# Kernel optimization log

Measured on AMD Instinct MI355X. Metric: run time of the kernel, lower is better.

## Reference

```python
import jax, jax.numpy as jnp
import numpy as np

B, S, IN, E, L = 8, 1024, 768, 256, 12

def setup_inputs() -> dict:
    key = jax.random.key(0)
    k1, k2, k3, k4 = jax.random.split(key, 4)
    input_tensor = jax.random.normal(k1, (B, S, IN), dtype=jnp.float32)
    fc_w = jax.random.normal(k2, (E, IN), dtype=jnp.float32) * (1.0 / np.sqrt(IN))
    fc_b = jax.random.normal(k3, (E,), dtype=jnp.float32) * 0.02
    bi_w = jax.random.normal(k4, (E * L, E), dtype=jnp.float32) * (1.0 / np.sqrt(E))
    bias = jnp.zeros((E,), dtype=jnp.float32)
    return {"input_tensor": input_tensor, "fc_w": fc_w, "fc_b": fc_b, "bi_w": bi_w, "bias": bias}

def reference(input_tensor, fc_w, fc_b, bi_w, bias):
    # fc: [B,S,IN] -> [B,S,E]
    t = jnp.einsum('bsi,ei->bse', input_tensor, fc_w) + fc_b
    # bi_linear: [B,S,E] -> [B,S,L,E], plus bias over E
    bl = jnp.einsum('bse,fe->bsf', t, bi_w).reshape(B, S, L, E) + bias
    # bilinear score: out[b,i,l,j] = sum_e bl[b,i,l,e] * t[b,j,e]
    # (avoids materializing the O(B*S*S*E) expanded value tensor)
    return jnp.einsum('bile,bje->bilj', bl, t)
```

## Files before the change

kernel.cpp:

```cpp
#include <hip/hip_runtime.h>
#include <hip/hip_bf16.h>

typedef __bf16 bf16_t;
typedef __bf16 bf16x8 __attribute__((ext_vector_type(8)));
typedef __bf16 bf16x4 __attribute__((ext_vector_type(4)));
typedef float f32x4 __attribute__((ext_vector_type(4)));

__global__ __launch_bounds__(256)
void cvt_all(const float* __restrict__ in, bf16_t* __restrict__ o_in,
             const float* __restrict__ fw, bf16_t* __restrict__ o_fw,
             const float* __restrict__ bw, bf16_t* __restrict__ o_bw) {
    int i = blockIdx.x * 256 + threadIdx.x;
    const float* s;
    bf16_t* d;
    int k;
    if (i < 786432)      { s = in; d = o_in; k = i; }
    else if (i < 811008) { s = fw; d = o_fw; k = i - 786432; }
    else if (i < 909312) { s = bw; d = o_bw; k = i - 811008; }
    else return;
    float4 a = ((const float4*)s)[k * 2];
    float4 b = ((const float4*)s)[k * 2 + 1];
    bf16x8 v;
    v[0] = (bf16_t)a.x; v[1] = (bf16_t)a.y; v[2] = (bf16_t)a.z; v[3] = (bf16_t)a.w;
    v[4] = (bf16_t)b.x; v[5] = (bf16_t)b.y; v[6] = (bf16_t)b.z; v[7] = (bf16_t)b.w;
    ((bf16x8*)d)[k] = v;
}

template <int BM, int BN, int EPI>
__global__ __launch_bounds__(256)
void gemm_bt(const bf16_t* __restrict__ A, const bf16_t* __restrict__ Bm,
             void* __restrict__ Cv, const float* __restrict__ bias,
             int M, int N, int K) {
    constexpr int MR = BM / 32;
    constexpr int NR = BN / 32;
    typedef float fvec __attribute__((ext_vector_type(NR)));
    typedef bf16_t bvec __attribute__((ext_vector_type(NR)));

    __shared__ bf16_t As[BM * 64];
    __shared__ bf16_t Bs[BN * 64];

    const int tid  = threadIdx.x;
    const int lane = tid & 63;
    const int wave = tid >> 6;
    const int mblk = blockIdx.x, nblk = blockIdx.y;

    const bf16_t* Ab = A + (long)mblk * BM * K;
    const bf16_t* Bb = Bm + (long)nblk * BN * K;

    f32x4 acc[MR][NR] = {};

    const int wrow = (wave >> 1) * (BM / 2);
    const int wcol = (wave & 1) * (BN / 2);
    const int lrow = lane & 15;
    const int kgrp = lane >> 4;

    for (int k0 = 0; k0 < K; k0 += 64) {
#pragma unroll
        for (int it = 0; it < MR; ++it) {
            const int chunk = it * 256 + tid;
            const int row = chunk >> 3, c8 = chunk & 7;
            __builtin_amdgcn_global_load_lds(
                (const __attribute__((address_space(1))) void*)(Ab + (long)row * K + k0 + c8 * 8),
                (__attribute__((address_space(3))) void*)(As + chunk * 8), 16, 0, 0);
        }
#pragma unroll
        for (int it = 0; it < NR; ++it) {
            const int chunk = it * 256 + tid;
            const int row = chunk >> 3, c8 = chunk & 7;
            __builtin_amdgcn_global_load_lds(
                (const __attribute__((address_space(1))) void*)(Bb + (long)row * K + k0 + c8 * 8),
                (__attribute__((address_space(3))) void*)(Bs + chunk * 8), 16, 0, 0);
        }
        __syncthreads();

#pragma unroll
        for (int kk = 0; kk < 64; kk += 32) {
            const int koff = kk + kgrp * 8;
            bf16x8 af[MR], bfr[NR];
#pragma unroll
            for (int m = 0; m < MR; ++m)
                af[m] = *(const bf16x8*)(As + (wrow + m * 16 + lrow) * 64 + koff);
#pragma unroll
            for (int n = 0; n < NR; ++n)
                bfr[n] = *(const bf16x8*)(Bs + (wcol + lrow * NR + n) * 64 + koff);
#pragma unroll
            for (int m = 0; m < MR; ++m)
#pragma unroll
                for (int n = 0; n < NR; ++n)
                    acc[m][n] = __builtin_amdgcn_mfma_f32_16x16x32_bf16(af[m], bfr[n], acc[m][n], 0, 0, 0);
        }
        __syncthreads();
    }

    const long rbase = (long)mblk * BM + wrow + kgrp * 4;
    const long cb0   = (long)nblk * BN + wcol + lrow * NR;
    bf16_t* C = (bf16_t*)Cv;
    const float* bp = bias + cb0;
    fvec bv = *(const fvec*)bp;
#pragma unroll
    for (int m = 0; m < MR; ++m)
#pragma unroll
        for (int j = 0; j < 4; ++j) {
            bvec v;
#pragma unroll
            for (int n = 0; n < NR; ++n) v[n] = (bf16_t)(acc[m][n][j] + bv[n]);
            *(bvec*)(C + (rbase + m * 16 + j) * N + cb0) = v;
        }
}

template <int EPI, int XCD, int NMB, int NNB>
__global__ __launch_bounds__(512, 2)
void gemm8p(const bf16_t* __restrict__ A, const bf16_t* __restrict__ Bm,
            void* __restrict__ Cv, const float* __restrict__ bias,
            int N, long sA, long sB, long sC) {
    constexpr int K = 256;
    extern __shared__ bf16_t lds[];

    const int tid  = threadIdx.x;
    const int lane = tid & 63;
    const int wave = tid >> 6;
    const int wm = wave >> 2, wn = wave & 3;
    const int lrow = lane & 15, kgrp = lane >> 4;

    int mblk, nblk, bz;
    {
        int L = blockIdx.x;
        if (XCD) { bz = L & 7; int w = L >> 3; nblk = w % NNB; mblk = w / NNB; }
        else     { bz = 0;     mblk = L % NMB; nblk = L / NMB; }
    }

    const bf16_t* Ab = A + (long)bz * sA + (long)mblk * 256 * K;
    const bf16_t* Bb = Bm + (long)bz * sB + (long)nblk * 256 * K;

    const int c0 = tid, c1 = 512 + tid;
    const int r0 = c0 >> 3, r1 = c1 >> 3;
    const int ca0 = (c0 & 7) ^ (r0 & 7),        ca1 = (c1 & 7) ^ (r1 & 7);
    const int cb0 = (c0 & 7) ^ ((r0 >> 2) & 7), cb1 = (c1 & 7) ^ ((r1 >> 2) & 7);

    auto stageA = [&](int t, int h) {
        const bf16_t* s0 = Ab + (long)(h * 128 + r0) * K + t * 64 + ca0 * 8;
        const bf16_t* s1 = Ab + (long)(h * 128 + r1) * K + t * 64 + ca1 * 8;
        bf16_t* d = lds + ((t & 1) * 2 + h) * 8192;
        __builtin_amdgcn_global_load_lds((const __attribute__((address_space(1))) void*)s0,
            (__attribute__((address_space(3))) void*)(d + c0 * 8), 16, 0, 0);
        __builtin_amdgcn_global_load_lds((const __attribute__((address_space(1))) void*)s1,
            (__attribute__((address_space(3))) void*)(d + c1 * 8), 16, 0, 0);
    };
    auto stageB = [&](int t, int h) {
        const bf16_t* s0 = Bb + (long)(h * 128 + r0) * K + t * 64 + cb0 * 8;
        const bf16_t* s1 = Bb + (long)(h * 128 + r1) * K + t * 64 + cb1 * 8;
        bf16_t* d = lds + 32768 + ((t & 1) * 2 + h) * 8192;
        __builtin_amdgcn_global_load_lds((const __attribute__((address_space(1))) void*)s0,
            (__attribute__((address_space(3))) void*)(d + c0 * 8), 16, 0, 0);
        __builtin_amdgcn_global_load_lds((const __attribute__((address_space(1))) void*)s1,
            (__attribute__((address_space(3))) void*)(d + c1 * 8), 16, 0, 0);
    };
    auto ldA = [&](int t, int mf, int kk) -> bf16x8 {
        const int row = mf * 16 + lrow;
        const int col = (kk * 32 + kgrp * 8) ^ ((row & 7) << 3);
        return *(const bf16x8*)(lds + ((t & 1) * 2 + wm) * 8192 + row * 64 + col);
    };
    auto ldB = [&](int t, int g, int kk) -> bf16x8 {
        const int row = (wn & 1) * 64 + lrow * 4 + g;
        const int col = (kk * 32 + kgrp * 8) ^ (((row >> 2) & 7) << 3);
        return *(const bf16x8*)(lds + 32768 + ((t & 1) * 2 + (wn >> 1)) * 8192 + row * 64 + col);
    };

    f32x4 acc[8][4] = {};
    bf16x8 bfr[4][2];

    stageA(0, 0); stageA(0, 1); stageB(0, 0); stageB(0, 1); stageB(1, 0); stageB(1, 1);
    asm volatile("s_waitcnt vmcnt(4)" ::: "memory");
    __builtin_amdgcn_s_barrier();

#pragma unroll
    for (int i = 0; i < 2; ++i) {
#pragma unroll
        for (int p = 0; p < 8; ++p) {
            const int q = p & 3;
            const int t = 2 * i + (p >> 2);
            bf16x8 af[2][2];
            if (q == 0) {
#pragma unroll
                for (int g = 0; g < 4; ++g) { bfr[g][0] = ldB(t, g, 0); bfr[g][1] = ldB(t, g, 1); }
            }
#pragma unroll
            for (int mm = 0; mm < 2; ++mm) { af[mm][0] = ldA(t, 2 * q + mm, 0); af[mm][1] = ldA(t, 2 * q + mm, 1); }

            if (p == 0) stageA(2 * i + 1, 0);
            else if (p == 1) stageA(2 * i + 1, 1);
            else if (p == 2) { if (2 * i + 2 < 4) stageB(2 * i + 2, 0); }
            else if (p == 3) { if (2 * i + 2 < 4) stageB(2 * i + 2, 1); }
            else if (p == 4) { if (2 * i + 2 < 4) stageA(2 * i + 2, 0); }
            else if (p == 5) { if (2 * i + 2 < 4) stageA(2 * i + 2, 1); }
            else if (p == 6) { if (2 * i + 3 < 4) stageB(2 * i + 3, 0); }
            else             { if (2 * i + 3 < 4) stageB(2 * i + 3, 1); }

            __builtin_amdgcn_s_barrier();
            asm volatile("s_waitcnt lgkmcnt(0)" ::: "memory");
            __builtin_amdgcn_s_setprio(1);
#pragma unroll
            for (int mm = 0; mm < 2; ++mm)
#pragma unroll
                for (int g = 0; g < 4; ++g)
#pragma unroll
                    for (int kk = 0; kk < 2; ++kk)
                        acc[2 * q + mm][g] = __builtin_amdgcn_mfma_f32_16x16x32_bf16(
                            af[mm][kk], bfr[g][kk], acc[2 * q + mm][g], 0, 0, 0);
            __builtin_amdgcn_s_setprio(0);

            if (p == 3) {
                if (2 * i + 2 < 4) asm volatile("s_waitcnt vmcnt(4)" ::: "memory");
                else               asm volatile("s_waitcnt vmcnt(0)" ::: "memory");
            } else if (p == 7) {
                if (2 * i + 2 < 4) asm volatile("s_waitcnt vmcnt(4)" ::: "memory");
            }
            __builtin_amdgcn_s_barrier();
        }
    }

    const long rb = (long)mblk * 256 + wm * 128 + kgrp * 4;
    const long cb = (long)nblk * 256 + wn * 64 + lrow * 4;
    if constexpr (EPI == 0) {
        float* C = (float*)Cv + (long)bz * sC;
#pragma unroll
        for (int m = 0; m < 8; ++m)
#pragma unroll
            for (int j = 0; j < 4; ++j) {
                f32x4 v = { acc[m][0][j], acc[m][1][j], acc[m][2][j], acc[m][3][j] };
                __builtin_nontemporal_store(v, (f32x4*)(C + (rb + m * 16 + j) * N + cb));
            }
    } else {
        bf16_t* C = (bf16_t*)Cv;
        f32x4 bv = *(const f32x4*)(bias + (int)(cb & 255));
#pragma unroll
        for (int m = 0; m < 8; ++m)
#pragma unroll
            for (int j = 0; j < 4; ++j) {
                bf16x4 v;
#pragma unroll
                for (int g = 0; g < 4; ++g) v[g] = (bf16_t)(acc[m][g][j] + bv[g]);
                *(bf16x4*)(C + (rb + m * 16 + j) * N + cb) = v;
            }
    }
}

template <int NNB>
__global__ __launch_bounds__(256, 2)
void gemm3k(const bf16_t* __restrict__ A, const bf16_t* __restrict__ Bm,
            float* __restrict__ C, long sA, long sB, long sC) {
    constexpr int K = 256, BM = 192, BN = 128;
    extern __shared__ bf16_t lds[];

    const int tid  = threadIdx.x;
    const int lane = tid & 63;
    const int wave = tid >> 6;
    const int wm = wave >> 1, wn = wave & 1;
    const int lrow = lane & 15, kgrp = lane >> 4;

    const int L = blockIdx.x;
    const int bz = L & 7;
    const int w = L >> 3;
    const int nblk = w & (NNB - 1), mblk = w / NNB;

    const bf16_t* Ab = A + (long)bz * sA + (long)mblk * BM * K;
    const bf16_t* Bb = Bm + (long)bz * sB + (long)nblk * BN * K;

    auto stage = [&](int t) {
        const int buf = t & 1;
#pragma unroll
        for (int it = 0; it < 6; ++it) {
            const int c = it * 256 + tid, row = c >> 3;
            const int sa = (c & 7) ^ (row & 7);
            __builtin_amdgcn_global_load_lds(
                (const __attribute__((address_space(1))) void*)(Ab + (long)row * K + t * 64 + sa * 8),
                (__attribute__((address_space(3))) void*)(lds + buf * 12288 + c * 8), 16, 0, 0);
        }
#pragma unroll
        for (int it = 0; it < 4; ++it) {
            const int c = it * 256 + tid, row = c >> 3;
            const int sb = (c & 7) ^ ((row >> 2) & 7);
            __builtin_amdgcn_global_load_lds(
                (const __attribute__((address_space(1))) void*)(Bb + (long)row * K + t * 64 + sb * 8),
                (__attribute__((address_space(3))) void*)(lds + 24576 + buf * 8192 + c * 8), 16, 0, 0);
        }
    };

    f32x4 acc[6][4] = {};

    stage(0);
    __syncthreads();

#pragma unroll
    for (int t = 0; t < 4; ++t) {
        if (t < 3) stage(t + 1);
        const int buf = t & 1;
        bf16x8 af[6][2], bfr[4][2];
#pragma unroll
        for (int m = 0; m < 6; ++m) {
            const int r = wm * 96 + m * 16 + lrow;
#pragma unroll
            for (int kk = 0; kk < 2; ++kk)
                af[m][kk] = *(const bf16x8*)(lds + buf * 12288 + r * 64 +
                                             ((kk * 32 + kgrp * 8) ^ ((r & 7) << 3)));
        }
#pragma unroll
        for (int g = 0; g < 4; ++g) {
            const int r = wn * 64 + lrow * 4 + g;
#pragma unroll
            for (int kk = 0; kk < 2; ++kk)
                bfr[g][kk] = *(const bf16x8*)(lds + 24576 + buf * 8192 + r * 64 +
                                              ((kk * 32 + kgrp * 8) ^ (((r >> 2) & 7) << 3)));
        }
        __builtin_amdgcn_s_setprio(1);
#pragma unroll
        for (int m = 0; m < 6; ++m)
#pragma unroll
            for (int g = 0; g < 4; ++g)
#pragma unroll
                for (int kk = 0; kk < 2; ++kk)
                    acc[m][g] = __builtin_amdgcn_mfma_f32_16x16x32_bf16(
                        af[m][kk], bfr[g][kk], acc[m][g], 0, 0, 0);
        __builtin_amdgcn_s_setprio(0);
        __syncthreads();
    }

    float* Cb = C + (long)bz * sC;
    const long rb = (long)mblk * BM + wm * 96 + kgrp * 4;
    const long cb = (long)nblk * BN + wn * 64 + lrow * 4;
#pragma unroll
    for (int m = 0; m < 6; ++m)
#pragma unroll
        for (int j = 0; j < 4; ++j) {
            f32x4 v = { acc[m][0][j], acc[m][1][j], acc[m][2][j], acc[m][3][j] };
            __builtin_nontemporal_store(v, (f32x4*)(Cb + (rb + m * 16 + j) * 1024 + cb));
        }
}

extern "C" void kernel_launch(void* const* d_in, const int* in_sizes, int n_in,
                              void* d_out, int out_size, void* d_ws, size_t ws_size,
                              hipStream_t stream) {
    const float* input = (const float*)d_in[0];
    const float* fc_w  = (const float*)d_in[1];
    const float* fc_b  = (const float*)d_in[2];
    const float* bi_w  = (const float*)d_in[3];
    const float* bias  = (const float*)d_in[4];

    char* ws = (char*)d_ws;
    bf16_t* inA = (bf16_t*)(ws);
    bf16_t* wfc = (bf16_t*)(ws + 12582912);
    bf16_t* wbi = (bf16_t*)(ws + 12976128);
    bf16_t* t   = (bf16_t*)(ws + 14548992);
    bf16_t* bl  = (bf16_t*)(ws + 18743296);

    cvt_all<<<dim3(3552), dim3(256), 0, stream>>>(input, inA, fc_w, wfc, bi_w, wbi);

    gemm_bt<64, 64, 1><<<dim3(128, 4), dim3(256), 0, stream>>>(
        inA, wfc, (void*)t, fc_b, 8192, 256, 768);

    gemm8p<2, 0, 32, 12><<<dim3(384), dim3(512), 131072, stream>>>(
        t, wbi, (void*)bl, bias, 3072, 0L, 0L, 0L);

    gemm3k<8><<<dim3(4096), dim3(256), 81920, stream>>>(
        bl, t, (float*)d_out,
        (long)12288 * 256, (long)1024 * 256, (long)12288 * 1024);
}
```

Before: 125.0 us.

## Make final GEMM persistent per A row-panel, streaming all B column tiles

The final batched GEMM now has each block load a 96x256 panel of bl into LDS once. The block then loops over all eight 128-column tiles of t, double-buffering B through LDS, and writes each output tile before resetting its accumulators. This removes the repeated A reloads across column blocks and cuts the grid from 4096 to 1024 blocks, at the cost of smaller per-wave tiles (3x4 MFMA fragments) and a barrier on every k-step. The first fc GEMM's tile is also changed from 64 to 128 rows, which halves its grid.

```diff
diff --git a/kernel.cpp b/kernel.cpp
--- a/kernel.cpp
+++ b/kernel.cpp
@@ -5,6 +5,9 @@
 typedef __bf16 bf16x8 __attribute__((ext_vector_type(8)));
 typedef __bf16 bf16x4 __attribute__((ext_vector_type(4)));
 typedef float f32x4 __attribute__((ext_vector_type(4)));
+
+#define AS1 __attribute__((address_space(1)))
+#define AS3 __attribute__((address_space(3)))
 
 __global__ __launch_bounds__(256)
 void cvt_all(const float* __restrict__ in, bf16_t* __restrict__ o_in,
@@ -60,16 +63,16 @@
             const int chunk = it * 256 + tid;
             const int row = chunk >> 3, c8 = chunk & 7;
             __builtin_amdgcn_global_load_lds(
-                (const __attribute__((address_space(1))) void*)(Ab + (long)row * K + k0 + c8 * 8),
-                (__attribute__((address_space(3))) void*)(As + chunk * 8), 16, 0, 0);
+                (const AS1 void*)(Ab + (long)row * K + k0 + c8 * 8),
+                (AS3 void*)(As + chunk * 8), 16, 0, 0);
         }
 #pragma unroll
         for (int it = 0; it < NR; ++it) {
             const int chunk = it * 256 + tid;
             const int row = chunk >> 3, c8 = chunk & 7;
             __builtin_amdgcn_global_load_lds(
-                (const __attribute__((address_space(1))) void*)(Bb + (long)row * K + k0 + c8 * 8),
-                (__attribute__((address_space(3))) void*)(Bs + chunk * 8), 16, 0, 0);
+                (const AS1 void*)(Bb + (long)row * K + k0 + c8 * 8),
+                (AS3 void*)(Bs + chunk * 8), 16, 0, 0);
         }
         __syncthreads();
 
@@ -141,19 +144,15 @@
         const bf16_t* s0 = Ab + (long)(h * 128 + r0) * K + t * 64 + ca0 * 8;
         const bf16_t* s1 = Ab + (long)(h * 128 + r1) * K + t * 64 + ca1 * 8;
         bf16_t* d = lds + ((t & 1) * 2 + h) * 8192;
-        __builtin_amdgcn_global_load_lds((const __attribute__((address_space(1))) void*)s0,
-            (__attribute__((address_space(3))) void*)(d + c0 * 8), 16, 0, 0);
-        __builtin_amdgcn_global_load_lds((const __attribute__((address_space(1))) void*)s1,
-            (__attribute__((address_space(3))) void*)(d + c1 * 8), 16, 0, 0);
+        __builtin_amdgcn_global_load_lds((const AS1 void*)s0, (AS3 void*)(d + c0 * 8), 16, 0, 0);
+        __builtin_amdgcn_global_load_lds((const AS1 void*)s1, (AS3 void*)(d + c1 * 8), 16, 0, 0);
     };
     auto stageB = [&](int t, int h) {
         const bf16_t* s0 = Bb + (long)(h * 128 + r0) * K + t * 64 + cb0 * 8;
         const bf16_t* s1 = Bb + (long)(h * 128 + r1) * K + t * 64 + cb1 * 8;
         bf16_t* d = lds + 32768 + ((t & 1) * 2 + h) * 8192;
-        __builtin_amdgcn_global_load_lds((const __attribute__((address_space(1))) void*)s0,
-            (__attribute__((address_space(3))) void*)(d + c0 * 8), 16, 0, 0);
-        __builtin_amdgcn_global_load_lds((const __attribute__((address_space(1))) void*)s1,
-            (__attribute__((address_space(3))) void*)(d + c1 * 8), 16, 0, 0);
+        __builtin_amdgcn_global_load_lds((const AS1 void*)s0, (AS3 void*)(d + c0 * 8), 16, 0, 0);
+        __builtin_amdgcn_global_load_lds((const AS1 void*)s1, (AS3 void*)(d + c1 * 8), 16, 0, 0);
     };
     auto ldA = [&](int t, int mf, int kk) -> bf16x8 {
         const int row = mf * 16 + lrow;
@@ -245,12 +244,12 @@
     }
 }
 
-template <int NNB>
 __global__ __launch_bounds__(256, 2)
-void gemm3k(const bf16_t* __restrict__ A, const bf16_t* __restrict__ Bm,
+void gemm3p(const bf16_t* __restrict__ A, const bf16_t* __restrict__ Bm,
             float* __restrict__ C, long sA, long sB, long sC) {
-    constexpr int K = 256, BM = 192, BN = 128;
     extern __shared__ bf16_t lds[];
+    bf16_t* Alds = lds;
+    bf16_t* Blds = lds + 24576;
 
     const int tid  = threadIdx.x;
     const int lane = tid & 63;
@@ -260,81 +259,95 @@
 
     const int L = blockIdx.x;
     const int bz = L & 7;
-    const int w = L >> 3;
-    const int nblk = w & (NNB - 1), mblk = w / NNB;
-
-    const bf16_t* Ab = A + (long)bz * sA + (long)mblk * BM * K;
-    const bf16_t* Bb = Bm + (long)bz * sB + (long)nblk * BN * K;
-
-    auto stage = [&](int t) {
-        const int buf = t & 1;
-#pragma unroll
-        for (int it = 0; it < 6; ++it) {
-            const int c = it * 256 + tid, row = c >> 3;
-            const int sa = (c & 7) ^ (row & 7);
-            __builtin_amdgcn_global_load_lds(
-                (const __attribute__((address_space(1))) void*)(Ab + (long)row * K + t * 64 + sa * 8),
-                (__attribute__((address_space(3))) void*)(lds + buf * 12288 + c * 8), 16, 0, 0);
-        }
+    const int mblk = L >> 3;
+
+    const bf16_t* Ab = A + (long)bz * sA + (long)mblk * 96 * 256;
+    const bf16_t* Bb = Bm + (long)bz * sB;
+
+    auto stageB = [&](int s) {
+        const int nb2 = s >> 2, t2 = s & 3, buf = s & 1;
+        const bf16_t* base = Bb + (long)nb2 * 128 * 256;
 #pragma unroll
         for (int it = 0; it < 4; ++it) {
             const int c = it * 256 + tid, row = c >> 3;
             const int sb = (c & 7) ^ ((row >> 2) & 7);
             __builtin_amdgcn_global_load_lds(
-                (const __attribute__((address_space(1))) void*)(Bb + (long)row * K + t * 64 + sb * 8),
-                (__attribute__((address_space(3))) void*)(lds + 24576 + buf * 8192 + c * 8), 16, 0, 0);
-        }
-    };
-
-    f32x4 acc[6][4] = {};
-
-    stage(0);
-    __syncthreads();
-
-#pragma unroll
-    for (int t = 0; t < 4; ++t) {
-        if (t < 3) stage(t + 1);
-        const int buf = t & 1;
-        bf16x8 af[6][2], bfr[4][2];
-#pragma unroll
-        for (int m = 0; m < 6; ++m) {
-            const int r = wm * 96 + m * 16 + lrow;
-#pragma unroll
-            for (int kk = 0; kk < 2; ++kk)
-                af[m][kk] = *(const bf16x8*)(lds + buf * 12288 + r * 64 +
-                                             ((kk * 32 + kgrp * 8) ^ ((r & 7) << 3)));
-        }
-#pragma unroll
-        for (int g = 0; g < 4; ++g) {
-            const int r = wn * 64 + lrow * 4 + g;
-#pragma unroll
-            for (int kk = 0; kk < 2; ++kk)
-                bfr[g][kk] = *(const bf16x8*)(lds + 24576 + buf * 8192 + r * 64 +
-                                              ((kk * 32 + kgrp * 8) ^ (((r >> 2) & 7) << 3)));
-        }
-        __builtin_amdgcn_s_setprio(1);
-#pragma unroll
-        for (int m = 0; m < 6; ++m)
-#pragma unroll
-            for (int g = 0; g < 4; ++g)
+                (const AS1 void*)(base + (long)row * 256 + t2 * 64 + sb * 8),
+                (AS3 void*)(Blds + buf * 8192 + c * 8), 16, 0, 0);
+        }
+    };
+
+#pragma unroll
+    for (int it = 0; it < 12; ++it) {
+        const int c = it * 256 + tid;
+        const int row = c >> 5, c8 = c & 31;
+        const int s8 = c8 ^ (row & 7);
+        __builtin_amdgcn_global_load_lds(
+            (const AS1 void*)(Ab + (long)row * 256 + s8 * 8),
+            (AS3 void*)(Alds + c * 8), 16, 0, 0);
+    }
+    stageB(0);
+    asm volatile("s_waitcnt vmcnt(0)" ::: "memory");
+    __builtin_amdgcn_s_barrier();
+
+    f32x4 acc[3][4] = {};
+    float* Cb = C + (long)bz * sC;
+    const long rb = (long)mblk * 96 + wm * 48 + kgrp * 4;
+
+    for (int nb = 0; nb < 8; ++nb) {
+#pragma unroll
+        for (int t = 0; t < 4; ++t) {
+            const int s = nb * 4 + t;
+            if (s < 31) stageB(s + 1);
+
+            bf16x8 af[3][2], bfr[4][2];
+#pragma unroll
+            for (int m = 0; m < 3; ++m) {
+                const int r = wm * 48 + m * 16 + lrow;
+#pragma unroll
+                for (int kk = 0; kk < 2; ++kk) {
+                    const int g8 = t * 8 + kk * 4 + kgrp;
+                    af[m][kk] = *(const bf16x8*)(Alds + r * 256 + (g8 ^ (r & 7)) * 8);
+                }
+            }
+#pragma unroll
+            for (int g = 0; g < 4; ++g) {
+                const int r = wn * 64 + lrow * 4 + g;
 #pragma unroll
                 for (int kk = 0; kk < 2; ++kk)
-                    acc[m][g] = __builtin_amdgcn_mfma_f32_16x16x32_bf16(
-                        af[m][kk], bfr[g][kk], acc[m][g], 0, 0, 0);
-        __builtin_amdgcn_s_setprio(0);
-        __syncthreads();
-    }
-
-    float* Cb = C + (long)bz * sC;
-    const long rb = (long)mblk * BM + wm * 96 + kgrp * 4;
-    const long cb = (long)nblk * BN + wn * 64 + lrow * 4;
-#pragma unroll
-    for (int m = 0; m < 6; ++m)
-#pragma unroll
-        for (int j = 0; j < 4; ++j) {
-            f32x4 v = { acc[m][0][j], acc[m][1][j], acc[m][2][j], acc[m][3][j] };
-            __builtin_nontemporal_store(v, (f32x4*)(Cb + (rb + m * 16 + j) * 1024 + cb));
-        }
+                    bfr[g][kk] = *(const bf16x8*)(Blds + (t & 1) * 8192 + r * 64 +
+                                                  ((kk * 32 + kgrp * 8) ^ (((r >> 2) & 7) << 3)));
+            }
+
+            __builtin_amdgcn_s_setprio(1);
+#pragma unroll
+            for (int m = 0; m < 3; ++m)
+#pragma unroll
+                for (int g = 0; g < 4; ++g)
+#pragma unroll
+                    for (int kk = 0; kk < 2; ++kk)
+                        acc[m][g] = __builtin_amdgcn_mfma_f32_16x16x32_bf16(
+                            af[m][kk], bfr[g][kk], acc[m][g], 0, 0, 0);
+            __builtin_amdgcn_s_setprio(0);
+
+            if (t == 3) {
+                const long cb = (long)nb * 128 + wn * 64 + lrow * 4;
+#pragma unroll
+                for (int m = 0; m < 3; ++m)
+#pragma unroll
+                    for (int j = 0; j < 4; ++j) {
+                        f32x4 v = { acc[m][0][j], acc[m][1][j], acc[m][2][j], acc[m][3][j] };
+                        __builtin_nontemporal_store(v, (f32x4*)(Cb + (rb + m * 16 + j) * 1024 + cb));
+                    }
+#pragma unroll
+                for (int m = 0; m < 3; ++m)
+#pragma unroll
+                    for (int g = 0; g < 4; ++g)
+                        acc[m][g] = f32x4{0.f, 0.f, 0.f, 0.f};
+            }
+            __syncthreads();
+        }
+    }
 }
 
 extern "C" void kernel_launch(void* const* d_in, const int* in_sizes, int n_in,
@@ -355,13 +368,13 @@
 
     cvt_all<<<dim3(3552), dim3(256), 0, stream>>>(input, inA, fc_w, wfc, bi_w, wbi);
 
-    gemm_bt<64, 64, 1><<<dim3(128, 4), dim3(256), 0, stream>>>(
+    gemm_bt<128, 64, 1><<<dim3(64, 4), dim3(256), 0, stream>>>(
         inA, wfc, (void*)t, fc_b, 8192, 256, 768);
 
     gemm8p<2, 0, 32, 12><<<dim3(384), dim3(512), 131072, stream>>>(
         t, wbi, (void*)bl, bias, 3072, 0L, 0L, 0L);
 
-    gemm3k<8><<<dim3(4096), dim3(256), 81920, stream>>>(
+    gemm3p<<<dim3(1024), dim3(256), 81920, stream>>>(
         bl, t, (float*)d_out,
         (long)12288 * 256, (long)1024 * 256, (long)12288 * 1024);
 }
```

Result: slower. 131.2 us (+5.0%).
